# Optimization experiments

Hardware: AMD Instinct MI355X
Metric: run time of the kernel (lower is better)

Reference implementation:

```python
import jax, jax.numpy as jnp
import numpy as np

T, B, D, H_DIM = 1024, 64, 512, 512
SIGMA = 0.01


def setup_inputs() -> dict:
    key = jax.random.key(0)
    ks = jax.random.split(key, 9)
    inp = {
        "inputs": jax.random.normal(ks[0], (T, B, D), dtype=jnp.float32),
        "W_xi": jax.random.normal(ks[1], (D, H_DIM), dtype=jnp.float32) * SIGMA,
        "W_hi": jax.random.normal(ks[2], (H_DIM, H_DIM), dtype=jnp.float32) * SIGMA,
        "b_i": jnp.zeros((H_DIM,), dtype=jnp.float32),
        "W_xf": jax.random.normal(ks[3], (D, H_DIM), dtype=jnp.float32) * SIGMA,
        "W_hf": jax.random.normal(ks[4], (H_DIM, H_DIM), dtype=jnp.float32) * SIGMA,
        "b_f": jnp.zeros((H_DIM,), dtype=jnp.float32),
        "W_xo": jax.random.normal(ks[5], (D, H_DIM), dtype=jnp.float32) * SIGMA,
        "W_ho": jax.random.normal(ks[6], (H_DIM, H_DIM), dtype=jnp.float32) * SIGMA,
        "b_o": jnp.zeros((H_DIM,), dtype=jnp.float32),
        "W_xc": jax.random.normal(ks[7], (D, H_DIM), dtype=jnp.float32) * SIGMA,
        "W_hc": jax.random.normal(ks[8], (H_DIM, H_DIM), dtype=jnp.float32) * SIGMA,
        "b_c": jnp.zeros((H_DIM,), dtype=jnp.float32),
    }
    return inp


def reference(inputs, W_xi, W_hi, b_i, W_xf, W_hf, b_f,
              W_xo, W_ho, b_o, W_xc, W_hc, b_c):
    # inputs: [T, B, D]. Precompute input-to-gate projections in one big
    # batched GEMM per gate (same math as per-step X @ W_x + b).
    Xi = jnp.einsum('tbd,dh->tbh', inputs, W_xi) + b_i
    Xf = jnp.einsum('tbd,dh->tbh', inputs, W_xf) + b_f
    Xo = jnp.einsum('tbd,dh->tbh', inputs, W_xo) + b_o
    Xc = jnp.einsum('tbd,dh->tbh', inputs, W_xc) + b_c

    Bsz = inputs.shape[1]
    H0 = jnp.zeros((Bsz, W_hi.shape[0]), dtype=inputs.dtype)
    C0 = jnp.zeros((Bsz, W_hi.shape[0]), dtype=inputs.dtype)

    def step(carry, xs):
        H, C = carry
        xi, xf, xo, xc = xs
        I = jax.nn.sigmoid(xi + H @ W_hi)
        F = jax.nn.sigmoid(xf + H @ W_hf)
        O = jax.nn.sigmoid(xo + H @ W_ho)
        C_tilde = jnp.tanh(xc + H @ W_hc)
        C = F * C + I * C_tilde
        H = O * jnp.tanh(C)
        return (H, C), H

    (H, C), outputs = jax.lax.scan(step, (H0, C0), (Xi, Xf, Xo, Xc))
    # outputs: [T, B, H] stacked hidden states (torch returns a list of them)
    return outputs, (H, C)
```

## Files before the change

kernel.cpp:

```cpp
#include <hip/hip_runtime.h>
#include <hip/hip_bf16.h>
#include <stdint.h>


typedef float    f32x4  __attribute__((ext_vector_type(4)));
typedef short    s16x8  __attribute__((ext_vector_type(8)));
typedef unsigned short u16;
typedef u16      u16x4  __attribute__((ext_vector_type(4)));
typedef unsigned int u32;

#define TT 1024
#define BB 64
#define DD 512
#define HH 512
#define NG 2048
#define NTEAM 8
#define NSLOT 8
#define NLW 128
#define NGEN 4

__device__ __forceinline__ u16 f2bf(float f) {
  __hip_bfloat16 h = __float2bfloat16(f);
  union { __hip_bfloat16 b; u16 u; } v; v.b = h; return v.u;
}
__device__ __forceinline__ float bf2f(u16 u) {
  union { unsigned int i; float f; } v; v.i = ((unsigned int)u) << 16; return v.f;
}
__device__ __forceinline__ float sig_fast(float x) { return 1.f / (1.f + __expf(-x)); }
__device__ __forceinline__ float tanh_fast(float x) { return 1.f - 2.f / (1.f + __expf(2.f * x)); }

__device__ __forceinline__ void gload_lds16(const u16* g, u16* l) {
  __builtin_amdgcn_global_load_lds(
      (const __attribute__((address_space(1))) unsigned int*)g,
      (__attribute__((address_space(3))) unsigned int*)l, 16, 0, 0);
}

__device__ __forceinline__ void st_plain(u32* p, u32 v) {
  asm volatile("global_store_dword %0, %1, off" :: "v"(p), "v"(v) : "memory");
}
__device__ __forceinline__ void st_dword_sc0(u32* p, u32 v) {
  asm volatile("global_store_dword %0, %1, off sc0" :: "v"(p), "v"(v) : "memory");
}
__device__ __forceinline__ void st_short_sc0(u16* p, u16 v) {
  asm volatile("global_store_short %0, %1, off sc0" :: "v"(p), "v"((u32)v) : "memory");
}
__device__ __forceinline__ u32 ld_plain(const u32* p) {
  u32 v;
  asm volatile("global_load_dword %0, %1, off\n\ts_waitcnt vmcnt(0)"
               : "=v"(v) : "v"(p) : "memory");
  return v;
}

__global__ void k_cast(const float* __restrict__ in, u16* __restrict__ out, long n) {
  long i = ((long)blockIdx.x * blockDim.x + threadIdx.x) * 4;
  if (i >= n) return;
  const float4 v = *(const float4*)(in + i);
  u16x4 o; o.x = f2bf(v.x); o.y = f2bf(v.y); o.z = f2bf(v.z); o.w = f2bf(v.w);
  *(u16x4*)(out + i) = o;
}

__global__ void k_pack(const float* __restrict__ Wxi, const float* __restrict__ Whi, const float* __restrict__ bi,
                       const float* __restrict__ Wxf, const float* __restrict__ Whf, const float* __restrict__ bfi,
                       const float* __restrict__ Wxo, const float* __restrict__ Who, const float* __restrict__ bo,
                       const float* __restrict__ Wxc, const float* __restrict__ Whc, const float* __restrict__ bc,
                       u16* __restrict__ WxT, u16* __restrict__ WhT, float* __restrict__ biasp)
{
  const int k = blockIdx.x;
  const float* Wx[4] = {Wxi, Wxf, Wxo, Wxc};
  const float* Wh[4] = {Whi, Whf, Who, Whc};
  for (int h = threadIdx.x; h < HH; h += blockDim.x) {
#pragma unroll
    for (int g = 0; g < 4; ++g) {
      const long n = h * 4 + g;
      WxT[n * DD + k] = f2bf(Wx[g][(long)k * HH + h]);
      WhT[n * HH + k] = f2bf(Wh[g][(long)k * HH + h]);
    }
  }
  if (k == 0) {
    const float* bp[4] = {bi, bfi, bo, bc};
    for (int n = threadIdx.x; n < NG; n += blockDim.x)
      biasp[n] = bp[n & 3][n >> 2];
  }
}

__global__ __launch_bounds__(256) void k_gemm_x(
    const u16* __restrict__ A, const u16* __restrict__ BT,
    const float* __restrict__ biasp, u16* __restrict__ X)
{
  __shared__ __align__(16) u16 As[128 * 64];
  __shared__ __align__(16) u16 Bs[128 * 64];
  const int tid = threadIdx.x;
  const int l = tid & 63;
  const int w = tid >> 6;
  const int wr = w >> 1, wc = w & 1;
  const long brow = (long)blockIdx.y * 128;
  const int  bcol = blockIdx.x * 128;
  const int  lr = l >> 3, lc = l & 7;
  const int  cl = l & 15, rg = l >> 4;

  f32x4 acc[4][4];
#pragma unroll
  for (int m = 0; m < 4; ++m)
#pragma unroll
    for (int n = 0; n < 4; ++n) acc[m][n] = (f32x4){0.f, 0.f, 0.f, 0.f};

  for (int k0 = 0; k0 < DD; k0 += 64) {
#pragma unroll
    for (int j = 0; j < 4; ++j) {
      const int sub = w * 4 + j;
      gload_lds16(A  + (brow + sub * 8 + lr) * DD + k0 + lc * 8, &As[sub * 512]);
      gload_lds16(BT + ((long)(bcol + sub * 8 + lr)) * DD + k0 + lc * 8, &Bs[sub * 512]);
    }
    __syncthreads();
#pragma unroll
    for (int kk = 0; kk < 2; ++kk) {
      s16x8 af[4], bfr[4];
#pragma unroll
      for (int m = 0; m < 4; ++m)
        af[m] = *(const s16x8*)&As[(wr * 64 + m * 16 + cl) * 64 + kk * 32 + rg * 8];
#pragma unroll
      for (int n = 0; n < 4; ++n)
        bfr[n] = *(const s16x8*)&Bs[(wc * 64 + n * 16 + cl) * 64 + kk * 32 + rg * 8];
#pragma unroll
      for (int m = 0; m < 4; ++m)
#pragma unroll
        for (int n = 0; n < 4; ++n)
          acc[m][n] = __builtin_amdgcn_mfma_f32_16x16x32_bf16(af[m], bfr[n], acc[m][n], 0, 0, 0);
    }
    __syncthreads();
  }
#pragma unroll
  for (int n = 0; n < 4; ++n) {
    const int col = bcol + wc * 64 + n * 16 + cl;
    const float bv = biasp[col];
#pragma unroll
    for (int m = 0; m < 4; ++m)
#pragma unroll
      for (int j = 0; j < 4; ++j) {
        const long row = brow + wr * 64 + m * 16 + rg * 4 + j;
        X[row * NG + col] = f2bf(acc[m][n][j] + bv);
      }
  }
}

__global__ __launch_bounds__(512, 2) void k_lstm(
    const u16* __restrict__ X, const u16* __restrict__ WhT,
    u16* __restrict__ Hh, float* __restrict__ Cst,
    float* __restrict__ dout, float* __restrict__ doutH, float* __restrict__ doutC,
    u32* __restrict__ ctl, u32* __restrict__ flags, int t0, int t1)
{
  __shared__ __align__(16) float pre[8][260];
  __shared__ int s_team, s_slot, s_mixed;
  const int tid = threadIdx.x;

  if (tid == 0) {
    u32 x;
    asm volatile("s_getreg_b32 %0, hwreg(HW_REG_XCC_ID)" : "=s"(x));
    x &= 7u;
    u32 r = __hip_atomic_fetch_add(&ctl[x], 1u, __ATOMIC_RELAXED, __HIP_MEMORY_SCOPE_AGENT);
    u32 p = 0;
    if (r >= NSLOT)
      p = __hip_atomic_fetch_add(&ctl[8], 1u, __ATOMIC_RELAXED, __HIP_MEMORY_SCOPE_AGENT);
    __hip_atomic_fetch_add(&ctl[9], 1u, __ATOMIC_RELAXED, __HIP_MEMORY_SCOPE_AGENT);
    while (__hip_atomic_load(&ctl[9], __ATOMIC_RELAXED, __HIP_MEMORY_SCOPE_AGENT) < (u32)NLW)
      __builtin_amdgcn_s_sleep(4);
    u32 c[8];
#pragma unroll
    for (int i = 0; i < 8; ++i)
      c[i] = __hip_atomic_load(&ctl[i], __ATOMIC_RELAXED, __HIP_MEMORY_SCOPE_AGENT);
    int team = -1, slot = 0;
    if (r < NSLOT) { team = (int)x; slot = (int)r; }
    else {
      u32 acc = 0;
      for (int tt = 0; tt < 8; ++tt) {
        u32 have = c[tt] < NSLOT ? c[tt] : NSLOT;
        u32 miss = NSLOT - have;
        if (team < 0 && p < acc + miss) { team = tt; slot = (int)(have + (p - acc)); }
        acc += miss;
      }
    }
    s_team = team; s_slot = slot;
    s_mixed = (team >= 0 && c[team] < NSLOT) ? 1 : 0;
  }
  __syncthreads();
  const int team = s_team, slot = s_slot, mixed = s_mixed;
  if (team < 0) return;

  const int l = tid & 63, wv = tid >> 6;
  const int cl = l & 15, rg = l >> 4;
  const int gcol0 = slot * 256 + wv * 32;

  s16x8 bfr[2][16];
#pragma unroll
  for (int nt = 0; nt < 2; ++nt)
#pragma unroll
    for (int ks = 0; ks < 16; ++ks)
      bfr[nt][ks] = *(const s16x8*)&WhT[(long)(gcol0 + nt * 16 + cl) * HH + ks * 32 + rg * 8];

  const int prow = tid >> 6;
  const int phl  = tid & 63;
  const int grow = team * 8 + prow;
  const int ghl  = slot * 64 + phl;

  float creg;
  if (t0 == 0) creg = 0.f; else creg = Cst[grow * HH + ghl];

  u32* fteam = flags + (long)team * TT * NGEN * 32;

  for (int t = t0; t < t1; ++t) {
    const int s = t - t0;
    u16x4 xv = *(const u16x4*)&X[((long)s * BB + grow) * NG + slot * 256 + phl * 4];

    if (t > t0) {
      if (wv == 0) {
        u32* fstep = fteam + (long)(s - 1) * NGEN * 32;
        u32 vv; unsigned long long b;
        int g = 0;
        for (;;) {
          if (l < NSLOT) vv = ld_plain(fstep + g * 32 + l);
          else vv = 1u;
          b = __ballot(vv != 0);
          if (b == ~0ULL) break;
          ++g;
          if (g >= NGEN) break;
          __builtin_amdgcn_s_sleep(2);
        }
        while (b != ~0ULL) {
          __builtin_amdgcn_s_sleep(8);
          if (l < NSLOT)
            vv = __hip_atomic_load(fstep + l, __ATOMIC_RELAXED, __HIP_MEMORY_SCOPE_AGENT);
          else vv = 1u;
          b = __ballot(vv != 0);
        }
      }
      __syncthreads();
    }

    f32x4 a0a = (f32x4){0.f,0.f,0.f,0.f}, a0b = (f32x4){0.f,0.f,0.f,0.f};
    f32x4 a1a = (f32x4){0.f,0.f,0.f,0.f}, a1b = (f32x4){0.f,0.f,0.f,0.f};
    if (t > 0) {
      const u16* Hp = Hh + (long)(t - 1) * BB * HH;
      s16x8 af[16];
#pragma unroll
      for (int ks = 0; ks < 16; ++ks) af[ks] = (s16x8){0,0,0,0,0,0,0,0};
      if (cl < 8) {
#pragma unroll
        for (int ks = 0; ks < 16; ++ks)
          af[ks] = *(const s16x8*)&Hp[(team * 8 + cl) * HH + ks * 32 + rg * 8];
      }
#pragma unroll
      for (int ks = 0; ks < 16; ks += 2) {
        a0a = __builtin_amdgcn_mfma_f32_16x16x32_bf16(af[ks],     bfr[0][ks],     a0a, 0, 0, 0);
        a1a = __builtin_amdgcn_mfma_f32_16x16x32_bf16(af[ks],     bfr[1][ks],     a1a, 0, 0, 0);
        a0b = __builtin_amdgcn_mfma_f32_16x16x32_bf16(af[ks + 1], bfr[0][ks + 1], a0b, 0, 0, 0);
        a1b = __builtin_amdgcn_mfma_f32_16x16x32_bf16(af[ks + 1], bfr[1][ks + 1], a1b, 0, 0, 0);
      }
    }
    const f32x4 acc0 = a0a + a0b, acc1 = a1a + a1b;
    if (rg < 2) {
#pragma unroll
      for (int j = 0; j < 4; ++j) {
        pre[rg * 4 + j][wv * 32 + cl]      = acc0[j];
        pre[rg * 4 + j][wv * 32 + 16 + cl] = acc1[j];
      }
    }
    __syncthreads();

    f32x4 pv = *(const f32x4*)&pre[prow][phl * 4];
    const float pi = pv[0] + bf2f((u16)xv.x);
    const float pf = pv[1] + bf2f((u16)xv.y);
    const float po = pv[2] + bf2f((u16)xv.z);
    const float pc = pv[3] + bf2f((u16)xv.w);
    const float ig = sig_fast(pi);
    const float fg = sig_fast(pf);
    const float og = sig_fast(po);
    const float ct = tanh_fast(pc);
    creg = fg * creg + ig * ct;
    const float hv = og * tanh_fast(creg);
    const u16 hb = f2bf(hv);
    u16* hdst = &Hh[((long)t * BB + grow) * HH + ghl];
    if (!mixed) st_short_sc0(hdst, hb);
    else asm volatile("global_store_short %0, %1, off sc1"
                      :: "v"(hdst), "v"((u32)hb) : "memory");

    asm volatile("s_waitcnt vmcnt(0)" ::: "memory");
    __syncthreads();
    if (tid == 0) {
      u32* fb = fteam + (long)s * NGEN * 32 + slot;
      if (!mixed) {
#pragma unroll
        for (int g = 0; g < NGEN; ++g) st_dword_sc0(fb + g * 32, 1u);
      } else {
#pragma unroll
        for (int g = 0; g < NGEN; ++g)
          __hip_atomic_store(fb + g * 32, 1u, __ATOMIC_RELAXED,
                             __HIP_MEMORY_SCOPE_AGENT);
      }
    }
    dout[((long)t * BB + grow) * HH + ghl] = hv;
    if (t == TT - 1) {
      doutH[grow * HH + ghl] = hv;
      doutC[grow * HH + ghl] = creg;
    }
  }

  Cst[grow * HH + ghl] = creg;
}

extern "C" void kernel_launch(void* const* d_in, const int* in_sizes, int n_in,
                              void* d_out, int out_size, void* d_ws, size_t ws_size,
                              hipStream_t stream)
{
  const float* inputs = (const float*)d_in[0];
  const float* W_xi = (const float*)d_in[1];
  const float* W_hi = (const float*)d_in[2];
  const float* b_i  = (const float*)d_in[3];
  const float* W_xf = (const float*)d_in[4];
  const float* W_hf = (const float*)d_in[5];
  const float* b_f  = (const float*)d_in[6];
  const float* W_xo = (const float*)d_in[7];
  const float* W_ho = (const float*)d_in[8];
  const float* b_o  = (const float*)d_in[9];
  const float* W_xc = (const float*)d_in[10];
  const float* W_hc = (const float*)d_in[11];
  const float* b_c  = (const float*)d_in[12];
  float* out = (float*)d_out;
  char* ws = (char*)d_ws;

  size_t off = 0;
  auto walloc = [&](size_t sz) { size_t o = off; off = (off + sz + 255) & ~(size_t)255; return o; };
  const size_t o_inbf  = walloc((size_t)TT * BB * DD * 2);
  const size_t o_WxT   = walloc((size_t)NG * DD * 2);
  const size_t o_WhT   = walloc((size_t)NG * HH * 2);
  const size_t o_bias  = walloc((size_t)NG * 4);
  const size_t o_C     = walloc((size_t)BB * HH * 4);
  const size_t o_Hh    = walloc((size_t)TT * BB * HH * 2);
  const size_t o_ctl   = walloc(256);
  const size_t flags_bytes = (size_t)NTEAM * TT * NGEN * 32 * 4;
  const size_t o_flags = walloc(flags_bytes);
  const size_t o_X     = off;

  const size_t bytes_per_step = (size_t)BB * NG * 2;
  long spc = (ws_size > o_X) ? (long)((ws_size - o_X) / bytes_per_step) : 0;
  if (spc > TT) spc = TT;
  spc &= ~1L;
  if (spc < 2) spc = 2;

  u16*   inbf  = (u16*)(ws + o_inbf);
  u16*   WxT   = (u16*)(ws + o_WxT);
  u16*   WhT   = (u16*)(ws + o_WhT);
  float* biasp = (float*)(ws + o_bias);
  u16*   Xbuf  = (u16*)(ws + o_X);
  u16*   Hh    = (u16*)(ws + o_Hh);
  float* Cst   = (float*)(ws + o_C);

  k_cast<<<dim3((TT * BB * DD) / 1024), dim3(256), 0, stream>>>(inputs, inbf, (long)TT * BB * DD);
  k_pack<<<dim3(DD), dim3(256), 0, stream>>>(W_xi, W_hi, b_i, W_xf, W_hf, b_f,
                                             W_xo, W_ho, b_o, W_xc, W_hc, b_c,
                                             WxT, WhT, biasp);

  float* doutH = out + (size_t)TT * BB * HH;
  float* doutC = doutH + (size_t)BB * HH;

  for (int t0 = 0; t0 < TT; t0 += (int)spc) {
    int t1 = t0 + (int)spc; if (t1 > TT) t1 = TT;
    const int rows = (t1 - t0) * BB;
    k_gemm_x<<<dim3(NG / 128, rows / 128), dim3(256), 0, stream>>>(
        inbf + (size_t)t0 * BB * DD, WxT, biasp, Xbuf);
    hipMemsetAsync(ws + o_ctl, 0, 256, stream);
    hipMemsetAsync(ws + o_flags, 0, flags_bytes, stream);
    k_lstm<<<dim3(NLW), dim3(512), 0, stream>>>(
        Xbuf, WhT, Hh, Cst, out, doutH, doutC,
        (u32*)(ws + o_ctl), (u32*)(ws + o_flags), t0, t1);
  }
}
```

Baseline: 4.376 ms.

## Rework inter-block step flags with more copies, backoff polling, and lane-parallel stores

Doubles the number of replicated flag copies per step and replaces the fixed polling loop with a graduated sleep backoff that walks through the copies, then falls back to atomic fetch-add polling. Flag writes are spread across lanes of wave 0 instead of a serial loop on thread 0, and each block pre-clears its next-step flag slots. The sc0 cache bits are dropped from the hidden-state and flag stores, and the output stores are moved before the wait and barrier. The goal is lower synchronization latency on the recurrent critical path. In exchange, the output stores now have to drain before the flag is published, and the weaker store cache bits could affect cross-block visibility.

```diff
diff --git a/kernel.cpp b/kernel.cpp
--- a/kernel.cpp
+++ b/kernel.cpp
@@ -17,7 +17,7 @@
 #define NTEAM 8
 #define NSLOT 8
 #define NLW 128
-#define NGEN 4
+#define NGEN 8
 
 __device__ __forceinline__ u16 f2bf(float f) {
   __hip_bfloat16 h = __float2bfloat16(f);
@@ -37,12 +37,6 @@
 
 __device__ __forceinline__ void st_plain(u32* p, u32 v) {
   asm volatile("global_store_dword %0, %1, off" :: "v"(p), "v"(v) : "memory");
-}
-__device__ __forceinline__ void st_dword_sc0(u32* p, u32 v) {
-  asm volatile("global_store_dword %0, %1, off sc0" :: "v"(p), "v"(v) : "memory");
-}
-__device__ __forceinline__ void st_short_sc0(u16* p, u16 v) {
-  asm volatile("global_store_short %0, %1, off sc0" :: "v"(p), "v"((u32)v) : "memory");
 }
 __device__ __forceinline__ u32 ld_plain(const u32* p) {
   u32 v;
@@ -206,6 +200,7 @@
   if (t0 == 0) creg = 0.f; else creg = Cst[grow * HH + ghl];
 
   u32* fteam = flags + (long)team * TT * NGEN * 32;
+  const int nsteps = t1 - t0;
 
   for (int t = t0; t < t1; ++t) {
     const int s = t - t0;
@@ -214,23 +209,28 @@
     if (t > t0) {
       if (wv == 0) {
         u32* fstep = fteam + (long)(s - 1) * NGEN * 32;
-        u32 vv; unsigned long long b;
         int g = 0;
-        for (;;) {
-          if (l < NSLOT) vv = ld_plain(fstep + g * 32 + l);
-          else vv = 1u;
-          b = __ballot(vv != 0);
-          if (b == ~0ULL) break;
+        auto touch = [&]() -> bool {
+          u32 vv = (l < NSLOT) ? ld_plain(fstep + g * 32 + l) : 1u;
+          unsigned long long b = __ballot(vv != 0);
           ++g;
-          if (g >= NGEN) break;
-          __builtin_amdgcn_s_sleep(2);
-        }
-        while (b != ~0ULL) {
+          return b == ~0ULL;
+        };
+        bool ok = touch();
+        if (!ok) { __builtin_amdgcn_s_sleep(1);  ok = touch(); }
+        if (!ok) { __builtin_amdgcn_s_sleep(2);  ok = touch(); }
+        if (!ok) { __builtin_amdgcn_s_sleep(4);  ok = touch(); }
+        if (!ok) { __builtin_amdgcn_s_sleep(4);  ok = touch(); }
+        if (!ok) { __builtin_amdgcn_s_sleep(8);  ok = touch(); }
+        if (!ok) { __builtin_amdgcn_s_sleep(8);  ok = touch(); }
+        if (!ok) { __builtin_amdgcn_s_sleep(16); ok = touch(); }
+        while (!ok) {
           __builtin_amdgcn_s_sleep(8);
-          if (l < NSLOT)
-            vv = __hip_atomic_load(fstep + l, __ATOMIC_RELAXED, __HIP_MEMORY_SCOPE_AGENT);
-          else vv = 1u;
-          b = __ballot(vv != 0);
+          u32 vv = (l < NSLOT)
+            ? __hip_atomic_fetch_add(fstep + l, 0u, __ATOMIC_RELAXED,
+                                     __HIP_MEMORY_SCOPE_AGENT)
+            : 1u;
+          ok = (__ballot(vv != 0) == ~0ULL);
         }
       }
       __syncthreads();
@@ -279,28 +279,24 @@
     const float hv = og * tanh_fast(creg);
     const u16 hb = f2bf(hv);
     u16* hdst = &Hh[((long)t * BB + grow) * HH + ghl];
-    if (!mixed) st_short_sc0(hdst, hb);
+    if (!mixed) *hdst = hb;
     else asm volatile("global_store_short %0, %1, off sc1"
                       :: "v"(hdst), "v"((u32)hb) : "memory");
 
-    asm volatile("s_waitcnt vmcnt(0)" ::: "memory");
-    __syncthreads();
-    if (tid == 0) {
-      u32* fb = fteam + (long)s * NGEN * 32 + slot;
-      if (!mixed) {
-#pragma unroll
-        for (int g = 0; g < NGEN; ++g) st_dword_sc0(fb + g * 32, 1u);
-      } else {
-#pragma unroll
-        for (int g = 0; g < NGEN; ++g)
-          __hip_atomic_store(fb + g * 32, 1u, __ATOMIC_RELAXED,
-                             __HIP_MEMORY_SCOPE_AGENT);
-      }
-    }
     dout[((long)t * BB + grow) * HH + ghl] = hv;
     if (t == TT - 1) {
       doutH[grow * HH + ghl] = hv;
       doutC[grow * HH + ghl] = creg;
+    }
+    asm volatile("s_waitcnt vmcnt(0)" ::: "memory");
+    __syncthreads();
+
+    if (wv == 0 && l < NGEN) {
+      u32* fb = fteam + (long)s * NGEN * 32 + l * 32 + slot;
+      if (!mixed) st_plain(fb, 1u);
+      else __hip_atomic_store(fb, 1u, __ATOMIC_RELAXED, __HIP_MEMORY_SCOPE_AGENT);
+      if (s + 1 < nsteps)
+        st_plain(fteam + (long)(s + 1) * NGEN * 32 + l * 32 + slot, 0u);
     }
   }
 
```

Result: no change. 4.313 ms (-1.4%).
